# Performance work log

Hardware: AMD Instinct MI355X
Metric: run time of the kernel (lower is better)

Reference implementation:

```python
import jax, jax.numpy as jnp
import numpy as np

B, N, E, H, F, L, S = 4, 384, 768, 32, 3072, 12, 512
D = E // H


def setup_inputs() -> dict:
    key = jax.random.key(0)
    ks = jax.random.split(key, 32)
    inp = {}
    # forward args
    inp['node_type'] = jax.random.randint(ks[0], (B, N, 1), 1, S + 1)  # table has S+1 rows; 0 = pad (unused)
    inp['node_input_feature'] = jax.random.normal(ks[1], (B, N, E), jnp.float32)
    inp['in_degree'] = jax.random.randint(ks[2], (B, N), 0, S)
    inp['out_degree'] = jax.random.randint(ks[3], (B, N), 0, S)
    inp['attn_bias'] = jax.random.normal(ks[4], (B, N, N), jnp.float32) * 0.1
    inp['spatial_pos'] = jax.random.randint(ks[5], (B, N, N), 0, S)
    # embedding tables (normal stddev 0.02, as in the flax module)
    inp['node_emb'] = jax.random.normal(ks[6], (S + 1, E), jnp.float32) * 0.02
    inp['in_deg_emb'] = jax.random.normal(ks[7], (S, E), jnp.float32) * 0.02
    inp['out_deg_emb'] = jax.random.normal(ks[8], (S, E), jnp.float32) * 0.02
    inp['sp_emb'] = jax.random.normal(ks[9], (S, H), jnp.float32) * 0.02
    inp['sp_emb_rev'] = jax.random.normal(ks[10], (S, H), jnp.float32) * 0.02
    # per-layer weights, stacked along leading L axis
    se, sf = 1.0 / np.sqrt(E), 1.0 / np.sqrt(F)
    inp['Wq'] = jax.random.normal(ks[11], (L, E, E), jnp.float32) * se
    inp['bq'] = jax.random.normal(ks[12], (L, E), jnp.float32) * se
    inp['Wk'] = jax.random.normal(ks[13], (L, E, E), jnp.float32) * se
    inp['bk'] = jax.random.normal(ks[14], (L, E), jnp.float32) * se
    inp['Wv'] = jax.random.normal(ks[15], (L, E, E), jnp.float32) * se
    inp['bv'] = jax.random.normal(ks[16], (L, E), jnp.float32) * se
    inp['Wo'] = jax.random.normal(ks[17], (L, E, E), jnp.float32) * se
    inp['bo'] = jnp.zeros((L, E), jnp.float32)
    inp['W1'] = jax.random.normal(ks[18], (L, E, F), jnp.float32) * se
    inp['b1'] = jax.random.normal(ks[19], (L, F), jnp.float32) * se
    inp['W2'] = jax.random.normal(ks[20], (L, F, E), jnp.float32) * sf
    inp['b2'] = jax.random.normal(ks[21], (L, E), jnp.float32) * sf
    inp['ln1_s'] = jnp.ones((L, E), jnp.float32)
    inp['ln1_b'] = jnp.zeros((L, E), jnp.float32)
    inp['ln2_s'] = jnp.ones((L, E), jnp.float32)
    inp['ln2_b'] = jnp.zeros((L, E), jnp.float32)
    return inp


def _layernorm(x, scale, bias, eps=1e-5):
    m = x.mean(-1, keepdims=True)
    v = ((x - m) ** 2).mean(-1, keepdims=True)
    return (x - m) / jnp.sqrt(v + eps) * scale + bias


def _encoder(node_type, node_input_feature, in_degree, out_degree, attn_bias, spatial_pos,
             node_emb, in_deg_emb, out_deg_emb, sp_emb, sp_emb_rev,
             Wq, bq, Wk, bk, Wv, bv, Wo, bo, W1, b1, W2, b2, ln1_s, ln1_b, ln2_s, ln2_b):
    nt = node_type[..., 0]                               # [B,N]
    padding_mask = nt == 0                               # [B,N]
    # node features: node_emb(node_type).sum(-2) + degree embeddings + input feature
    x = (node_emb[node_type].sum(axis=-2)
         + in_deg_emb[in_degree] + out_deg_emb[out_degree]
         + node_input_feature)                           # [B,N,E]
    # spatial attention bias: [B,N,N,H] -> [B,H,N,N], plus graph-level attn_bias
    sb = sp_emb[spatial_pos] + sp_emb_rev[jnp.transpose(spatial_pos, (0, 2, 1))]
    bias = jnp.transpose(sb, (0, 3, 1, 2)) + attn_bias[:, None]  # [B,H,N,N]

    x = jnp.transpose(x, (1, 0, 2))                      # [N,B,E]
    scaling = D ** (-0.5)
    neg_inf = jnp.float32(-jnp.inf)

    def layer(x, p):
        wq, bq_, wk, bk_, wv, bv_, wo, bo_, w1, b1_, w2, b2_, s1, t1, s2, t2 = p
        q = ((x @ wq) + bq_) * scaling                   # [N,B,E], bias scaled too (faithful)
        k = (x @ wk) + bk_
        v = (x @ wv) + bv_
        q = q.reshape(N, B, H, D)
        k = k.reshape(N, B, H, D)
        v = v.reshape(N, B, H, D)
        w = jnp.einsum('nbhd,mbhd->bhnm', q, k) + bias   # [B,H,N,N]
        w = jnp.where(padding_mask[:, None, None, :], neg_inf, w)
        probs = jax.nn.softmax(w.astype(jnp.float32), axis=-1).astype(x.dtype)
        a = jnp.einsum('bhnm,mbhd->nbhd', probs, v).reshape(N, B, E)
        a = a @ wo + bo_
        x = _layernorm(x + a, s1, t1)                    # post-LN
        h = jax.nn.gelu(x @ w1 + b1_)                    # approximate gelu (flax default)
        h = h @ w2 + b2_
        x = _layernorm(x + h, s2, t2)
        return x, None

    xs = (Wq, bq, Wk, bk, Wv, bv, Wo, bo, W1, b1, W2, b2, ln1_s, ln1_b, ln2_s, ln2_b)
    x, _ = jax.lax.scan(layer, x, xs)
    return x                                             # [N,B,E]


def reference(node_type, node_input_feature, in_degree, out_degree, attn_bias, spatial_pos,
              node_emb, in_deg_emb, out_deg_emb, sp_emb, sp_emb_rev,
              Wq, bq, Wk, bk, Wv, bv, Wo, bo, W1, b1, W2, b2, ln1_s, ln1_b, ln2_s, ln2_b):
    return _encoder(node_type, node_input_feature, in_degree, out_degree, attn_bias, spatial_pos,
                    node_emb, in_deg_emb, out_deg_emb, sp_emb, sp_emb_rev,
                    Wq, bq, Wk, bk, Wv, bv, Wo, bo, W1, b1, W2, b2, ln1_s, ln1_b, ln2_s, ln2_b)
```

## Files before the change

kernel.cpp:

```cpp
#include <hip/hip_runtime.h>
#include <hip/hip_bf16.h>

#define Bb 4
#define Nn 384
#define Ee 768
#define Hh 32
#define Ff 3072
#define Ll 12
#define Ss 512
#define Mm (Nn*Bb)

typedef __attribute__((ext_vector_type(8))) short bf16x8;
typedef __attribute__((ext_vector_type(4))) float f32x4;
typedef unsigned short u16;

__device__ __forceinline__ u16 f2b(float f) {
  union { float f; unsigned int i; } c; c.f = f;
  unsigned int x = c.i;
  return (u16)((x + 0x7fffu + ((x >> 16) & 1u)) >> 16);
}
__device__ __forceinline__ float b2f(u16 u) {
  union { unsigned int i; float f; } c; c.i = ((unsigned int)u) << 16; return c.f;
}
__device__ __forceinline__ unsigned pkcvt(float lo, float hi) {
  unsigned r;
  asm("v_cvt_pk_bf16_f32 %0, %1, %2" : "=v"(r) : "v"(lo), "v"(hi));
  return r;
}
__device__ __forceinline__ void gload_lds16(const void* g, void* l) {
  __builtin_amdgcn_global_load_lds((__attribute__((address_space(1))) void*)(g),
                                   (__attribute__((address_space(3))) void*)(l), 16, 0, 0);
}

__global__ __launch_bounds__(256) void embed_kernel(
    const int* __restrict__ node_type, const float* __restrict__ nif,
    const int* __restrict__ in_deg, const int* __restrict__ out_deg,
    const float* __restrict__ node_emb, const float* __restrict__ ind_emb,
    const float* __restrict__ outd_emb,
    float* __restrict__ x, u16* __restrict__ xb)
{
  const int r = blockIdx.x;
  const int n = r / Bb, b = r % Bb;
  const int nt  = node_type[b*Nn + n];
  const int idg = in_deg[b*Nn + n];
  const int odg = out_deg[b*Nn + n];
  for (int c = threadIdx.x; c < Ee; c += 256) {
    float val = node_emb[(size_t)nt*Ee + c] + ind_emb[(size_t)idg*Ee + c]
              + outd_emb[(size_t)odg*Ee + c] + nif[((size_t)b*Nn + n)*Ee + c];
    x[(size_t)r*Ee + c] = val;
    xb[(size_t)r*Ee + c] = f2b(val);
  }
}

__global__ void spT_kernel(const int* __restrict__ sp, int* __restrict__ spT)
{
  __shared__ int tile[32][33];
  const int b = blockIdx.z;
  const int n0 = blockIdx.y * 32, m0 = blockIdx.x * 32;
  const int tx = threadIdx.x, ty = threadIdx.y;
  for (int i = ty; i < 32; i += 8)
    tile[i][tx] = sp[((size_t)b*Nn + n0 + i)*Nn + m0 + tx];
  __syncthreads();
  for (int i = ty; i < 32; i += 8)
    spT[((size_t)b*Nn + m0 + i)*Nn + n0 + tx] = tile[tx][i];
}

__global__ __launch_bounds__(256) void bias_pre_kernel(
    const float* __restrict__ atb, const int* __restrict__ sp, const int* __restrict__ spT,
    const float* __restrict__ sp_emb, const float* __restrict__ sp_emb_rev,
    u16* __restrict__ biasb)
{
  __shared__ float spc[512], sprc[512];
  const int bx = blockIdx.x, h = blockIdx.y, b = blockIdx.z;
  const int t = threadIdx.x;
  for (int i = t; i < 512; i += 256) {
    spc[i]  = sp_emb[(size_t)i*Hh + h];
    sprc[i] = sp_emb_rev[(size_t)i*Hh + h];
  }
  __syncthreads();
  const int qi = t >> 4;
  const int ml = (t & 15) << 2;
  const size_t rowb = ((size_t)b*Nn + bx*16 + qi)*Nn;
  u16* outb = biasb + ((size_t)(b*Hh + h)*24 + bx)*24*256;
  #pragma unroll
  for (int mg = 0; mg < 6; ++mg) {
    const int m = mg*64 + ml;
    float4 a4 = *(const float4*)(atb + rowb + m);
    int4  s4 = *(const int4*)(sp  + rowb + m);
    int4  t4 = *(const int4*)(spT + rowb + m);
    const int tt = m >> 4, hi = (m >> 2) & 3;
    uint2 u;
    u.x = pkcvt(a4.x + spc[s4.x] + sprc[t4.x], a4.y + spc[s4.y] + sprc[t4.y]);
    u.y = pkcvt(a4.z + spc[s4.z] + sprc[t4.z], a4.w + spc[s4.w] + sprc[t4.w]);
    *(uint2*)(outb + tt*256 + hi*64 + qi*4) = u;
  }
}

__global__ __launch_bounds__(256) void wconv_kernel(
    const float* __restrict__ Wq, const float* __restrict__ Wk, const float* __restrict__ Wv,
    const float* __restrict__ Wo, const float* __restrict__ W1, const float* __restrict__ W2,
    int layer, u16* __restrict__ slot)
{
  __shared__ float tile[64][65];
  int tid = blockIdx.x;
  const float* src; u16* dst; int Ns, Ks;
  if (tid < 432)       { int seg = tid / 144; tid -= seg*144;
                         src = (seg==0?Wq:(seg==1?Wk:Wv)) + (size_t)layer*Ee*Ee;
                         dst = slot + (size_t)seg*589824; Ns = 768; Ks = 768; }
  else if (tid < 576)  { tid -= 432; src = Wo + (size_t)layer*Ee*Ee; dst = slot + 1769472; Ns = 768;  Ks = 768; }
  else if (tid < 1152) { tid -= 576; src = W1 + (size_t)layer*Ee*Ff; dst = slot + 2359296; Ns = 3072; Ks = 768; }
  else                 { tid -= 1152; src = W2 + (size_t)layer*Ff*Ee; dst = slot + 4718592; Ns = 768; Ks = 3072; }
  const int tc = Ns >> 6;
  const int tk = tid / tc, tn = tid % tc;
  const int t = threadIdx.x;
  #pragma unroll
  for (int i = 0; i < 4; ++i) {
    const int id = t + i*256;
    const int r = id >> 4, c = (id & 15) << 2;
    float4 v = *(const float4*)(src + (size_t)(tk*64 + r)*Ns + tn*64 + c);
    tile[r][c+0] = v.x; tile[r][c+1] = v.y; tile[r][c+2] = v.z; tile[r][c+3] = v.w;
  }
  __syncthreads();
  #pragma unroll
  for (int i = 0; i < 2; ++i) {
    const int ch = t + i*256;
    const int n = ch >> 3, kc = (ch & 7) << 3;
    uint4 u;
    u.x = pkcvt(tile[kc+0][n], tile[kc+1][n]);
    u.y = pkcvt(tile[kc+2][n], tile[kc+3][n]);
    u.z = pkcvt(tile[kc+4][n], tile[kc+5][n]);
    u.w = pkcvt(tile[kc+6][n], tile[kc+7][n]);
    *(uint4*)(dst + (size_t)(tn*64 + n)*Ks + tk*64 + kc) = u;
  }
}

template<int EPI>
__global__ __launch_bounds__(256) void gemm3_kernel(
    const u16* __restrict__ A, const u16* __restrict__ Bw,
    const float* __restrict__ b0, const float* __restrict__ b1, const float* __restrict__ b2,
    int Kfull, int Kc, float scaleQ,
    float* __restrict__ outF, u16* __restrict__ outB)
{
  __shared__ __align__(16) u16 As[2][128][64];
  __shared__ __align__(16) u16 Bs[2][64][64];
  const int t = threadIdx.x, lane = t & 63, wave = t >> 6;
  int bx = blockIdx.x, by = blockIdx.y;
  {
    const int gx = gridDim.x;
    const int nwg = gx * gridDim.y;
    const int bid = bx + gx * by;
    const int cpx = nwg >> 3;
    const int s = (bid & 7) * cpx + (bid >> 3);
    bx = s % gx; by = s / gx;
  }
  const int m0 = bx * 128, n0 = by * 64;
  const int k0 = blockIdx.z * Kc;
  const int wm = wave >> 1, wn = wave & 1;
  const int ql = lane & 15, hi = lane >> 4;
  const int nk = Kc >> 6;
  const int sr = t >> 3;
  const int sslot = (t & 7) ^ (sr & 7);
  const size_t aoff = (size_t)(m0 + sr)*Kfull + k0 + (sslot << 3);
  const size_t boff = (size_t)(n0 + sr)*Kfull + k0 + (sslot << 3);
  const size_t rstep = (size_t)32 * Kfull;

  int aro[4][2], bro[2][2];
  #pragma unroll
  for (int ks = 0; ks < 2; ++ks) {
    const int kb = (((ks<<2) + hi) ^ (ql & 7)) << 4;
    #pragma unroll
    for (int f = 0; f < 4; ++f) aro[f][ks] = (wm*64 + f*16 + ql)*128 + kb;
    #pragma unroll
    for (int f = 0; f < 2; ++f) bro[f][ks] = (wn*32 + f*16 + ql)*128 + kb;
  }

  f32x4 acc[4][2];
  #pragma unroll
  for (int a = 0; a < 4; ++a)
    #pragma unroll
    for (int c = 0; c < 2; ++c) acc[a][c] = (f32x4){0.f,0.f,0.f,0.f};

  #pragma unroll
  for (int i = 0; i < 4; ++i)
    gload_lds16(A + aoff + i*rstep, (char*)&As[0][0][0] + i*4096 + t*16);
  #pragma unroll
  for (int i = 0; i < 2; ++i)
    gload_lds16(Bw + boff + i*rstep, (char*)&Bs[0][0][0] + i*4096 + t*16);

  for (int kt = 0; kt < nk; ++kt) {
    const int cur = kt & 1, nxt = cur ^ 1;
    const bool pre = (kt + 1 < nk);
    if (pre) {
      const size_t kk = (size_t)(kt + 1) << 6;
      #pragma unroll
      for (int i = 0; i < 4; ++i)
        gload_lds16(A + aoff + kk + i*rstep, (char*)&As[nxt][0][0] + i*4096 + t*16);
      #pragma unroll
      for (int i = 0; i < 2; ++i)
        gload_lds16(Bw + boff + kk + i*rstep, (char*)&Bs[nxt][0][0] + i*4096 + t*16);
      asm volatile("s_waitcnt vmcnt(6)" ::: "memory");
    } else {
      asm volatile("s_waitcnt vmcnt(0)" ::: "memory");
    }
    __builtin_amdgcn_s_barrier();
    __builtin_amdgcn_sched_barrier(0);

    const char* aBase = (const char*)&As[cur][0][0];
    const char* bBase = (const char*)&Bs[cur][0][0];
    bf16x8 af[4][2], bf[2][2];
    #pragma unroll
    for (int f = 0; f < 4; ++f)
      #pragma unroll
      for (int ks = 0; ks < 2; ++ks)
        af[f][ks] = *(const bf16x8*)(aBase + aro[f][ks]);
    #pragma unroll
    for (int f = 0; f < 2; ++f)
      #pragma unroll
      for (int ks = 0; ks < 2; ++ks)
        bf[f][ks] = *(const bf16x8*)(bBase + bro[f][ks]);
    #pragma unroll
    for (int ks = 0; ks < 2; ++ks)
      #pragma unroll
      for (int fm = 0; fm < 4; ++fm)
        #pragma unroll
        for (int fn = 0; fn < 2; ++fn)
          acc[fm][fn] = __builtin_amdgcn_mfma_f32_16x16x32_bf16(af[fm][ks], bf[fn][ks], acc[fm][fn], 0, 0, 0);
    if (pre) {
      __builtin_amdgcn_sched_barrier(0);
      __builtin_amdgcn_s_barrier();
    }
  }

  #pragma unroll
  for (int fm = 0; fm < 4; ++fm) {
    const int rowb = m0 + wm*64 + fm*16 + hi*4;
    #pragma unroll
    for (int fn = 0; fn < 2; ++fn) {
      const int gcol = n0 + wn*32 + fn*16 + ql;
      float bv, scale = 1.0f;
      if (EPI == 0) {
        const int seg = gcol / 768;
        const int cw = gcol - seg*768;
        bv = (seg == 0) ? b0[cw] : ((seg == 1) ? b1[cw] : b2[cw]);
        if (seg == 0) scale = scaleQ;
      } else if (EPI == 1) {
        bv = (blockIdx.z == 0) ? b0[gcol] : 0.0f;
      } else {
        bv = b0[gcol];
      }
      f32x4 v = acc[fm][fn];
      #pragma unroll
      for (int j = 0; j < 4; ++j) {
        float val = (v[j] + bv) * scale;
        if (EPI == 0) {
          outB[(size_t)(rowb + j) * 2304 + gcol] = f2b(val);
        } else if (EPI == 1) {
          outF[(size_t)blockIdx.z * (Mm*768) + (size_t)(rowb + j) * 768 + gcol] = val;
        } else {
          float arg = 0.7978845608028654f * (val + 0.044715f * val * val * val);
          float e = __expf(2.0f * arg);
          float g = 0.5f * val * (2.0f - 2.0f / (e + 1.0f));
          outB[(size_t)(rowb + j) * 3072 + gcol] = f2b(g);
        }
      }
    }
  }
}

template<int PREBIAS>
__global__ __launch_bounds__(256) void attn2_kernel(
    const u16* __restrict__ qkv,
    const u16* __restrict__ biasb,
    const float* __restrict__ atb, const int* __restrict__ sp, const int* __restrict__ spT,
    const float* __restrict__ sp_emb, const float* __restrict__ sp_emb_rev,
    u16* __restrict__ ab)
{
  __shared__ __align__(16) u16 Kt[384][32];
  __shared__ __align__(16) u16 Vt[32][392];
  __shared__ __align__(16) u16 Qt[64][32];
  __shared__ __align__(16) u16 Pw[4][16][32];
  __shared__ float spc[512], sprc[512];
  const int bid = blockIdx.x;
  const int pair = bid % 3;
  const int h = (bid / 3) % Hh;
  const int b = bid / (3 * Hh);
  const int t = threadIdx.x, lane = t & 63, wave = t >> 6;
  const int ql = lane & 15, hi = lane >> 4;

  for (int idx = t; idx < 384*6; idx += 256) {
    const int m = idx / 6, c = idx - m*6;
    const u16* base = qkv + ((size_t)m*Bb + b)*2304 + h*24 + c*4;
    uint2 kk = *(const uint2*)(base + 768);
    uint2 vv = *(const uint2*)(base + 1536);
    *(uint2*)&Kt[m][c*4] = kk;
    Vt[c*4+0][m] = (u16)(vv.x & 0xffffu); Vt[c*4+1][m] = (u16)(vv.x >> 16);
    Vt[c*4+2][m] = (u16)(vv.y & 0xffffu); Vt[c*4+3][m] = (u16)(vv.y >> 16);
  }
  for (int idx = t; idx < 384*2; idx += 256)
    *(uint2*)&Kt[idx>>1][24 + (idx&1)*4] = make_uint2(0u, 0u);
  for (int idx = t; idx < 8*196; idx += 256)
    *(unsigned*)((char*)&Vt[24][0] + idx*4) = 0u;
  for (int idx = t; idx < 64*2; idx += 256)
    *(uint2*)&Qt[idx>>1][24 + (idx&1)*4] = make_uint2(0u, 0u);
  if (!PREBIAS) {
    for (int i = t; i < 512; i += 256) {
      spc[i]  = sp_emb[(size_t)i*Hh + h];
      sprc[i] = sp_emb_rev[(size_t)i*Hh + h];
    }
  }

  for (int qi = 0; qi < 2; ++qi) {
    const int ntile = pair*2 + qi;
    for (int idx = t; idx < 64*6; idx += 256) {
      const int qr = idx / 6, c = idx - qr*6;
      const u16* base = qkv + ((size_t)(ntile*64 + qr)*Bb + b)*2304 + h*24 + c*4;
      *(uint2*)&Qt[qr][c*4] = *(const uint2*)base;
    }
    __syncthreads();

    const int q0 = ntile*64 + wave*16;
    const int q = q0 + ql;
    const bf16x8 qf = *(const bf16x8*)&Qt[wave*16 + ql][hi*8];

    f32x4 f[24];
    const u16* bp = biasb + (((size_t)(b*Hh + h)*24 + ntile*4 + wave)*24)*256 + lane*4;
    const size_t crow = ((size_t)b*Nn + q)*Nn;
    #pragma unroll
    for (int tt = 0; tt < 24; ++tt) {
      bf16x8 kf = *(const bf16x8*)&Kt[tt*16 + ql][hi*8];
      f32x4 z = (f32x4){0.f,0.f,0.f,0.f};
      f32x4 s = __builtin_amdgcn_mfma_f32_16x16x32_bf16(kf, qf, z, 0, 0, 0);
      if (PREBIAS) {
        uint2 bb = *(const uint2*)(bp + tt*256);
        s[0] += b2f((u16)(bb.x & 0xffffu)); s[1] += b2f((u16)(bb.x >> 16));
        s[2] += b2f((u16)(bb.y & 0xffffu)); s[3] += b2f((u16)(bb.y >> 16));
      } else {
        const int off = tt*16 + hi*4;
        int4 s4 = *(const int4*)(sp + crow + off);
        int4 t4 = *(const int4*)(spT + crow + off);
        float4 a4 = *(const float4*)(atb + crow + off);
        s[0] += a4.x + spc[s4.x] + sprc[t4.x];
        s[1] += a4.y + spc[s4.y] + sprc[t4.y];
        s[2] += a4.z + spc[s4.z] + sprc[t4.z];
        s[3] += a4.w + spc[s4.w] + sprc[t4.w];
      }
      f[tt] = s;
    }

    float mx = -3.0e38f;
    #pragma unroll
    for (int tt = 0; tt < 24; ++tt)
      mx = fmaxf(mx, fmaxf(fmaxf(f[tt][0], f[tt][1]), fmaxf(f[tt][2], f[tt][3])));
    mx = fmaxf(mx, __shfl_xor(mx, 16, 64));
    mx = fmaxf(mx, __shfl_xor(mx, 32, 64));
    float sum = 0.f;
    #pragma unroll
    for (int tt = 0; tt < 24; ++tt) {
      #pragma unroll
      for (int j = 0; j < 4; ++j) { f[tt][j] = __expf(f[tt][j] - mx); sum += f[tt][j]; }
    }
    sum += __shfl_xor(sum, 16, 64);
    sum += __shfl_xor(sum, 32, 64);
    const float inv = 1.0f / sum;

    f32x4 o0 = (f32x4){0.f,0.f,0.f,0.f}, o1 = (f32x4){0.f,0.f,0.f,0.f};
    char* prow = (char*)&Pw[wave][ql][0];
    const int swz = (ql & 3) << 4;
    #pragma unroll
    for (int c = 0; c < 12; ++c) {
      unsigned w0 = pkcvt(f[2*c][0],   f[2*c][1]);
      unsigned w1 = pkcvt(f[2*c][2],   f[2*c][3]);
      unsigned w2 = pkcvt(f[2*c+1][0], f[2*c+1][1]);
      unsigned w3 = pkcvt(f[2*c+1][2], f[2*c+1][3]);
      *(unsigned*)(prow + (((hi*8)      ) ^ swz)) = w0;
      *(unsigned*)(prow + (((hi*8) +  4) ^ swz)) = w1;
      *(unsigned*)(prow + (((hi*8) + 32) ^ swz)) = w2;
      *(unsigned*)(prow + (((hi*8) + 36) ^ swz)) = w3;
      bf16x8 a = *(const bf16x8*)(prow + ((hi*16) ^ swz));
      bf16x8 v0 = *(const bf16x8*)&Vt[ql][c*32 + hi*8];
      bf16x8 v1 = *(const bf16x8*)&Vt[16 + ql][c*32 + hi*8];
      o0 = __builtin_amdgcn_mfma_f32_16x16x32_bf16(a, v0, o0, 0, 0, 0);
      o1 = __builtin_amdgcn_mfma_f32_16x16x32_bf16(a, v1, o1, 0, 0, 0);
    }

    #pragma unroll
    for (int j = 0; j < 4; ++j) {
      float invj = __shfl(inv, hi*4 + j, 64);
      const int qg = q0 + hi*4 + j;
      u16* orow = ab + ((size_t)qg*Bb + b)*Ee + h*24;
      orow[ql] = f2b(o0[j] * invj);
      if (ql < 8) orow[16 + ql] = f2b(o1[j] * invj);
    }
    __syncthreads();
  }
}

template<int NP>
__global__ __launch_bounds__(256) void ln_kernel(
    const float* __restrict__ xin, const float* __restrict__ delta,
    const float* __restrict__ gamma, const float* __restrict__ beta,
    float* __restrict__ xout, u16* __restrict__ xb)
{
  const int wave = threadIdx.x >> 6, lane = threadIdx.x & 63;
  const int r = blockIdx.x * 4 + wave;
  const size_t base = (size_t)r * Ee;
  const int c0 = lane * 12;
  float v[12];
  #pragma unroll
  for (int i = 0; i < 3; ++i) {
    float4 xv = *(const float4*)(xin + base + c0 + i*4);
    v[i*4+0] = xv.x; v[i*4+1] = xv.y; v[i*4+2] = xv.z; v[i*4+3] = xv.w;
  }
  #pragma unroll
  for (int p = 0; p < NP; ++p) {
    const float* dp = delta + (size_t)p*(Mm*768) + base + c0;
    #pragma unroll
    for (int i = 0; i < 3; ++i) {
      float4 dv = *(const float4*)(dp + i*4);
      v[i*4+0] += dv.x; v[i*4+1] += dv.y; v[i*4+2] += dv.z; v[i*4+3] += dv.w;
    }
  }
  float s = 0.f;
  #pragma unroll
  for (int i = 0; i < 12; ++i) s += v[i];
  #pragma unroll
  for (int off = 1; off < 64; off <<= 1) s += __shfl_xor(s, off, 64);
  const float mean = s * (1.0f / 768.0f);
  float qs = 0.f;
  #pragma unroll
  for (int i = 0; i < 12; ++i) { float d = v[i] - mean; qs += d * d; }
  #pragma unroll
  for (int off = 1; off < 64; off <<= 1) qs += __shfl_xor(qs, off, 64);
  const float rstd = rsqrtf(qs * (1.0f / 768.0f) + 1e-5f);
  float o[12];
  #pragma unroll
  for (int i = 0; i < 3; ++i) {
    float4 g4 = *(const float4*)(gamma + c0 + i*4);
    float4 b4 = *(const float4*)(beta + c0 + i*4);
    o[i*4+0] = (v[i*4+0] - mean) * rstd * g4.x + b4.x;
    o[i*4+1] = (v[i*4+1] - mean) * rstd * g4.y + b4.y;
    o[i*4+2] = (v[i*4+2] - mean) * rstd * g4.z + b4.z;
    o[i*4+3] = (v[i*4+3] - mean) * rstd * g4.w + b4.w;
    *(float4*)(xout + base + c0 + i*4) = make_float4(o[i*4+0], o[i*4+1], o[i*4+2], o[i*4+3]);
  }
  #pragma unroll
  for (int i = 0; i < 3; ++i) {
    uint2 u;
    u.x = pkcvt(o[i*4+0], o[i*4+1]);
    u.y = pkcvt(o[i*4+2], o[i*4+3]);
    *(uint2*)(xb + base + c0 + i*4) = u;
  }
}

extern "C" void kernel_launch(void* const* d_in, const int* in_sizes, int n_in,
                              void* d_out, int out_size, void* d_ws, size_t ws_size,
                              hipStream_t stream) {
  const int*   node_type  = (const int*)d_in[0];
  const float* nif        = (const float*)d_in[1];
  const int*   in_deg     = (const int*)d_in[2];
  const int*   out_deg    = (const int*)d_in[3];
  const float* atb        = (const float*)d_in[4];
  const int*   sp         = (const int*)d_in[5];
  const float* node_emb   = (const float*)d_in[6];
  const float* ind_emb    = (const float*)d_in[7];
  const float* outd_emb   = (const float*)d_in[8];
  const float* sp_emb     = (const float*)d_in[9];
  const float* sp_emb_rev = (const float*)d_in[10];
  const float* Wq = (const float*)d_in[11]; const float* bq = (const float*)d_in[12];
  const float* Wk = (const float*)d_in[13]; const float* bk = (const float*)d_in[14];
  const float* Wv = (const float*)d_in[15]; const float* bv = (const float*)d_in[16];
  const float* Wo = (const float*)d_in[17]; const float* bo = (const float*)d_in[18];
  const float* W1 = (const float*)d_in[19]; const float* b1 = (const float*)d_in[20];
  const float* W2 = (const float*)d_in[21]; const float* b2 = (const float*)d_in[22];
  const float* ln1s = (const float*)d_in[23]; const float* ln1b = (const float*)d_in[24];
  const float* ln2s = (const float*)d_in[25]; const float* ln2b = (const float*)d_in[26];

  char* ws = (char*)d_ws;
  float* x      = (float*)(ws);
  u16*   xb     = (u16*)(ws +  4718592);
  u16*   qkvb16 = (u16*)(ws +  7077888);
  u16*   abuf   = (u16*)(ws + 14155776);
  u16*   hb     = (u16*)(ws + 16515072);
  float* obufP  = (float*)(ws + 25952256);
  int*   spTb   = (int*)(ws + 44826624);
  u16*   biasb  = (u16*)(ws + 47185920);
  u16*   wTslot = (u16*)(ws + 84934656);
  const bool useBias = ws_size >= 99090432ull;

  embed_kernel<<<Mm, 256, 0, stream>>>(node_type, nif, in_deg, out_deg,
                                       node_emb, ind_emb, outd_emb, x, xb);
  spT_kernel<<<dim3(12, 12, 4), dim3(32, 8), 0, stream>>>(sp, spTb);
  if (useBias)
    bias_pre_kernel<<<dim3(24, 32, 4), 256, 0, stream>>>(atb, sp, spTb, sp_emb, sp_emb_rev, biasb);

  const float scaleQ = 0.2041241452319315f;

  for (int l = 0; l < Ll; ++l) {
    const float *bql = bq + (size_t)l*Ee, *bkl = bk + (size_t)l*Ee, *bvl = bv + (size_t)l*Ee;
    const float *bol = bo + (size_t)l*Ee;
    const float *b1l = b1 + (size_t)l*Ff, *b2l = b2 + (size_t)l*Ee;

    wconv_kernel<<<1728, 256, 0, stream>>>(Wq, Wk, Wv, Wo, W1, W2, l, wTslot);
    const u16* qkvT = wTslot;
    const u16* woT  = wTslot + 1769472;
    const u16* w1T  = wTslot + 2359296;
    const u16* w2T  = wTslot + 4718592;

    gemm3_kernel<0><<<dim3(12, 36), 256, 0, stream>>>(xb, qkvT, bql, bkl, bvl,
                                                      768, 768, scaleQ, nullptr, qkvb16);
    if (useBias)
      attn2_kernel<1><<<384, 256, 0, stream>>>(qkvb16, biasb, atb, sp, spTb,
                                               sp_emb, sp_emb_rev, abuf);
    else
      attn2_kernel<0><<<384, 256, 0, stream>>>(qkvb16, nullptr, atb, sp, spTb,
                                               sp_emb, sp_emb_rev, abuf);
    gemm3_kernel<1><<<dim3(12, 12, 2), 256, 0, stream>>>(abuf, woT, bol, bol, bol,
                                                         768, 384, 1.0f, obufP, nullptr);
    ln_kernel<2><<<Mm/4, 256, 0, stream>>>(x, obufP, ln1s + (size_t)l*Ee, ln1b + (size_t)l*Ee, x, xb);
    gemm3_kernel<2><<<dim3(12, 48), 256, 0, stream>>>(xb, w1T, b1l, b1l, b1l,
                                                      768, 768, 1.0f, nullptr, hb);
    gemm3_kernel<1><<<dim3(12, 12, 4), 256, 0, stream>>>(hb, w2T, b2l, b2l, b2l,
                                                         3072, 768, 1.0f, obufP, nullptr);
    float* xdst = (l == Ll - 1) ? (float*)d_out : x;
    ln_kernel<4><<<Mm/4, 256, 0, stream>>>(x, obufP, ln2s + (size_t)l*Ee, ln2b + (size_t)l*Ee, xdst, xb);
  }
}
```

Measured before the change: 1.291 ms.

## Fuse fp32 weight conversion and transpose into GEMM B-tile loads

Drops the per-layer wconv kernel that converted and transposed fp32 weights to bf16 in a workspace slot. Each GEMM now reads fp32 weights directly from global memory into registers, packs them to bf16 and writes them swizzled into LDS. This removes one launch and a round trip through the workspace per layer. In exchange, B tiles are loaded as 4-byte strided scalar reads instead of async direct-to-LDS loads, M-tile blocks re-convert the same weights, and a __syncthreads replaces the vmcnt-based pipelining.

```diff
diff --git a/kernel.cpp b/kernel.cpp
--- a/kernel.cpp
+++ b/kernel.cpp
@@ -96,49 +96,12 @@
   }
 }
 
-__global__ __launch_bounds__(256) void wconv_kernel(
-    const float* __restrict__ Wq, const float* __restrict__ Wk, const float* __restrict__ Wv,
-    const float* __restrict__ Wo, const float* __restrict__ W1, const float* __restrict__ W2,
-    int layer, u16* __restrict__ slot)
-{
-  __shared__ float tile[64][65];
-  int tid = blockIdx.x;
-  const float* src; u16* dst; int Ns, Ks;
-  if (tid < 432)       { int seg = tid / 144; tid -= seg*144;
-                         src = (seg==0?Wq:(seg==1?Wk:Wv)) + (size_t)layer*Ee*Ee;
-                         dst = slot + (size_t)seg*589824; Ns = 768; Ks = 768; }
-  else if (tid < 576)  { tid -= 432; src = Wo + (size_t)layer*Ee*Ee; dst = slot + 1769472; Ns = 768;  Ks = 768; }
-  else if (tid < 1152) { tid -= 576; src = W1 + (size_t)layer*Ee*Ff; dst = slot + 2359296; Ns = 3072; Ks = 768; }
-  else                 { tid -= 1152; src = W2 + (size_t)layer*Ff*Ee; dst = slot + 4718592; Ns = 768; Ks = 3072; }
-  const int tc = Ns >> 6;
-  const int tk = tid / tc, tn = tid % tc;
-  const int t = threadIdx.x;
-  #pragma unroll
-  for (int i = 0; i < 4; ++i) {
-    const int id = t + i*256;
-    const int r = id >> 4, c = (id & 15) << 2;
-    float4 v = *(const float4*)(src + (size_t)(tk*64 + r)*Ns + tn*64 + c);
-    tile[r][c+0] = v.x; tile[r][c+1] = v.y; tile[r][c+2] = v.z; tile[r][c+3] = v.w;
-  }
-  __syncthreads();
-  #pragma unroll
-  for (int i = 0; i < 2; ++i) {
-    const int ch = t + i*256;
-    const int n = ch >> 3, kc = (ch & 7) << 3;
-    uint4 u;
-    u.x = pkcvt(tile[kc+0][n], tile[kc+1][n]);
-    u.y = pkcvt(tile[kc+2][n], tile[kc+3][n]);
-    u.z = pkcvt(tile[kc+4][n], tile[kc+5][n]);
-    u.w = pkcvt(tile[kc+6][n], tile[kc+7][n]);
-    *(uint4*)(dst + (size_t)(tn*64 + n)*Ks + tk*64 + kc) = u;
-  }
-}
-
 template<int EPI>
-__global__ __launch_bounds__(256) void gemm3_kernel(
-    const u16* __restrict__ A, const u16* __restrict__ Bw,
+__global__ __launch_bounds__(256) void gemm5_kernel(
+    const u16* __restrict__ A,
+    const float* __restrict__ W0, const float* __restrict__ W1p, const float* __restrict__ W2p,
     const float* __restrict__ b0, const float* __restrict__ b1, const float* __restrict__ b2,
-    int Kfull, int Kc, float scaleQ,
+    int Kfull, int Ns, int Kc, float scaleQ,
     float* __restrict__ outF, u16* __restrict__ outB)
 {
   __shared__ __align__(16) u16 As[2][128][64];
@@ -158,11 +121,20 @@
   const int wm = wave >> 1, wn = wave & 1;
   const int ql = lane & 15, hi = lane >> 4;
   const int nk = Kc >> 6;
+  int n0loc = n0;
+  const float* Wsel = W0;
+  if (EPI == 0) {
+    const int seg = n0 / 768; n0loc = n0 - seg*768;
+    Wsel = (seg == 0) ? W0 : ((seg == 1) ? W1p : W2p);
+  }
   const int sr = t >> 3;
   const int sslot = (t & 7) ^ (sr & 7);
   const size_t aoff = (size_t)(m0 + sr)*Kfull + k0 + (sslot << 3);
-  const size_t boff = (size_t)(n0 + sr)*Kfull + k0 + (sslot << 3);
   const size_t rstep = (size_t)32 * Kfull;
+  const int bn = t & 63, kq = t >> 6;
+  const float* wb = Wsel + (size_t)(k0 + kq*16)*Ns + n0loc + bn;
+  const int bws0 = ((kq*2)     ^ (bn & 7)) << 4;
+  const int bws1 = ((kq*2 + 1) ^ (bn & 7)) << 4;
 
   int aro[4][2], bro[2][2];
   #pragma unroll
@@ -180,30 +152,37 @@
     #pragma unroll
     for (int c = 0; c < 2; ++c) acc[a][c] = (f32x4){0.f,0.f,0.f,0.f};
 
-  #pragma unroll
-  for (int i = 0; i < 4; ++i)
-    gload_lds16(A + aoff + i*rstep, (char*)&As[0][0][0] + i*4096 + t*16);
-  #pragma unroll
-  for (int i = 0; i < 2; ++i)
-    gload_lds16(Bw + boff + i*rstep, (char*)&Bs[0][0][0] + i*4096 + t*16);
+  {
+    #pragma unroll
+    for (int i = 0; i < 4; ++i)
+      gload_lds16(A + aoff + i*rstep, (char*)&As[0][0][0] + i*4096 + t*16);
+    float br[16];
+    #pragma unroll
+    for (int i = 0; i < 16; ++i) br[i] = wb[(size_t)i * Ns];
+    uint4 u0, u1;
+    u0.x = pkcvt(br[0],  br[1]);  u0.y = pkcvt(br[2],  br[3]);
+    u0.z = pkcvt(br[4],  br[5]);  u0.w = pkcvt(br[6],  br[7]);
+    u1.x = pkcvt(br[8],  br[9]);  u1.y = pkcvt(br[10], br[11]);
+    u1.z = pkcvt(br[12], br[13]); u1.w = pkcvt(br[14], br[15]);
+    char* bdst = (char*)&Bs[0][0][0] + bn*128;
+    *(uint4*)(bdst + bws0) = u0;
+    *(uint4*)(bdst + bws1) = u1;
+  }
+  __syncthreads();
 
   for (int kt = 0; kt < nk; ++kt) {
     const int cur = kt & 1, nxt = cur ^ 1;
     const bool pre = (kt + 1 < nk);
+    float br[16];
     if (pre) {
       const size_t kk = (size_t)(kt + 1) << 6;
       #pragma unroll
       for (int i = 0; i < 4; ++i)
         gload_lds16(A + aoff + kk + i*rstep, (char*)&As[nxt][0][0] + i*4096 + t*16);
-      #pragma unroll
-      for (int i = 0; i < 2; ++i)
-        gload_lds16(Bw + boff + kk + i*rstep, (char*)&Bs[nxt][0][0] + i*4096 + t*16);
-      asm volatile("s_waitcnt vmcnt(6)" ::: "memory");
-    } else {
-      asm volatile("s_waitcnt vmcnt(0)" ::: "memory");
-    }
-    __builtin_amdgcn_s_barrier();
-    __builtin_amdgcn_sched_barrier(0);
+      const float* wbt = wb + kk * Ns;
+      #pragma unroll
+      for (int i = 0; i < 16; ++i) br[i] = wbt[(size_t)i * Ns];
+    }
 
     const char* aBase = (const char*)&As[cur][0][0];
     const char* bBase = (const char*)&Bs[cur][0][0];
@@ -225,9 +204,17 @@
         #pragma unroll
         for (int fn = 0; fn < 2; ++fn)
           acc[fm][fn] = __builtin_amdgcn_mfma_f32_16x16x32_bf16(af[fm][ks], bf[fn][ks], acc[fm][fn], 0, 0, 0);
+
     if (pre) {
-      __builtin_amdgcn_sched_barrier(0);
-      __builtin_amdgcn_s_barrier();
+      uint4 u0, u1;
+      u0.x = pkcvt(br[0],  br[1]);  u0.y = pkcvt(br[2],  br[3]);
+      u0.z = pkcvt(br[4],  br[5]);  u0.w = pkcvt(br[6],  br[7]);
+      u1.x = pkcvt(br[8],  br[9]);  u1.y = pkcvt(br[10], br[11]);
+      u1.z = pkcvt(br[12], br[13]); u1.w = pkcvt(br[14], br[15]);
+      char* bdst = (char*)&Bs[nxt][0][0] + bn*128;
+      *(uint4*)(bdst + bws0) = u0;
+      *(uint4*)(bdst + bws1) = u1;
+      __syncthreads();
     }
   }
 
@@ -484,7 +471,6 @@
   float* obufP  = (float*)(ws + 25952256);
   int*   spTb   = (int*)(ws + 44826624);
   u16*   biasb  = (u16*)(ws + 47185920);
-  u16*   wTslot = (u16*)(ws + 84934656);
   const bool useBias = ws_size >= 99090432ull;
 
   embed_kernel<<<Mm, 256, 0, stream>>>(node_type, nif, in_deg, out_deg,
@@ -496,31 +482,28 @@
   const float scaleQ = 0.2041241452319315f;
 
   for (int l = 0; l < Ll; ++l) {
+    const float *wq = Wq + (size_t)l*Ee*Ee, *wk = Wk + (size_t)l*Ee*Ee, *wv = Wv + (size_t)l*Ee*Ee;
+    const float *wo = Wo + (size_t)l*Ee*Ee;
+    const float *w1 = W1 + (size_t)l*Ee*Ff, *w2 = W2 + (size_t)l*Ff*Ee;
     const float *bql = bq + (size_t)l*Ee, *bkl = bk + (size_t)l*Ee, *bvl = bv + (size_t)l*Ee;
     const float *bol = bo + (size_t)l*Ee;
     const float *b1l = b1 + (size_t)l*Ff, *b2l = b2 + (size_t)l*Ee;
 
-    wconv_kernel<<<1728, 256, 0, stream>>>(Wq, Wk, Wv, Wo, W1, W2, l, wTslot);
-    const u16* qkvT = wTslot;
-    const u16* woT  = wTslot + 1769472;
-    const u16* w1T  = wTslot + 2359296;
-    const u16* w2T  = wTslot + 4718592;
-
-    gemm3_kernel<0><<<dim3(12, 36), 256, 0, stream>>>(xb, qkvT, bql, bkl, bvl,
-                                                      768, 768, scaleQ, nullptr, qkvb16);
+    gemm5_kernel<0><<<dim3(12, 36), 256, 0, stream>>>(xb, wq, wk, wv, bql, bkl, bvl,
+                                                      768, 768, 768, scaleQ, nullptr, qkvb16);
     if (useBias)
       attn2_kernel<1><<<384, 256, 0, stream>>>(qkvb16, biasb, atb, sp, spTb,
                                                sp_emb, sp_emb_rev, abuf);
     else
       attn2_kernel<0><<<384, 256, 0, stream>>>(qkvb16, nullptr, atb, sp, spTb,
                                                sp_emb, sp_emb_rev, abuf);
-    gemm3_kernel<1><<<dim3(12, 12, 2), 256, 0, stream>>>(abuf, woT, bol, bol, bol,
-                                                         768, 384, 1.0f, obufP, nullptr);
+    gemm5_kernel<1><<<dim3(12, 12, 2), 256, 0, stream>>>(abuf, wo, wo, wo, bol, bol, bol,
+                                                         768, 768, 384, 1.0f, obufP, nullptr);
     ln_kernel<2><<<Mm/4, 256, 0, stream>>>(x, obufP, ln1s + (size_t)l*Ee, ln1b + (size_t)l*Ee, x, xb);
-    gemm3_kernel<2><<<dim3(12, 48), 256, 0, stream>>>(xb, w1T, b1l, b1l, b1l,
-                                                      768, 768, 1.0f, nullptr, hb);
-    gemm3_kernel<1><<<dim3(12, 12, 4), 256, 0, stream>>>(hb, w2T, b2l, b2l, b2l,
-                                                         3072, 768, 1.0f, obufP, nullptr);
+    gemm5_kernel<2><<<dim3(12, 48), 256, 0, stream>>>(xb, w1, w1, w1, b1l, b1l, b1l,
+                                                      768, 3072, 768, 1.0f, nullptr, hb);
+    gemm5_kernel<1><<<dim3(12, 12, 4), 256, 0, stream>>>(hb, w2, w2, w2, b2l, b2l, b2l,
+                                                         3072, 768, 768, 1.0f, obufP, nullptr);
     float* xdst = (l == Ll - 1) ? (float*)d_out : x;
     ln_kernel<4><<<Mm/4, 256, 0, stream>>>(x, obufP, ln2s + (size_t)l*Ee, ln2b + (size_t)l*Ee, xdst, xb);
   }
```

After: 1.436 ms. 1.11x slower.

## Use 64-row GEMM tiles for Wo/W2, drop split-K, fold residual into epilogue

Applied to the files above, without the earlier changes.

Templates the GEMM on an M-fragment count so the Wo and W2 projections use 64-row tiles with more blocks in M. This replaces split-K 2 with no split for Wo and cuts W2 split-K from 4 to 2. The residual x is added in the split-0 epilogue, so the layernorm reads fewer partial buffers and no longer reads x separately. The aim is less partial-sum traffic and better occupancy, at the cost of lower per-block data reuse in the GEMM.

```diff
diff --git a/kernel.cpp b/kernel.cpp
--- a/kernel.cpp
+++ b/kernel.cpp
@@ -134,14 +134,16 @@
   }
 }
 
-template<int EPI>
+template<int EPI, int FM>
 __global__ __launch_bounds__(256) void gemm3_kernel(
     const u16* __restrict__ A, const u16* __restrict__ Bw,
     const float* __restrict__ b0, const float* __restrict__ b1, const float* __restrict__ b2,
+    const float* __restrict__ resid,
     int Kfull, int Kc, float scaleQ,
     float* __restrict__ outF, u16* __restrict__ outB)
 {
-  __shared__ __align__(16) u16 As[2][128][64];
+  constexpr int MR = FM * 32;
+  __shared__ __align__(16) u16 As[2][MR][64];
   __shared__ __align__(16) u16 Bs[2][64][64];
   const int t = threadIdx.x, lane = t & 63, wave = t >> 6;
   int bx = blockIdx.x, by = blockIdx.y;
@@ -153,7 +155,7 @@
     const int s = (bid & 7) * cpx + (bid >> 3);
     bx = s % gx; by = s / gx;
   }
-  const int m0 = bx * 128, n0 = by * 64;
+  const int m0 = bx * MR, n0 = by * 64;
   const int k0 = blockIdx.z * Kc;
   const int wm = wave >> 1, wn = wave & 1;
   const int ql = lane & 15, hi = lane >> 4;
@@ -164,24 +166,24 @@
   const size_t boff = (size_t)(n0 + sr)*Kfull + k0 + (sslot << 3);
   const size_t rstep = (size_t)32 * Kfull;
 
-  int aro[4][2], bro[2][2];
+  int aro[FM][2], bro[2][2];
   #pragma unroll
   for (int ks = 0; ks < 2; ++ks) {
     const int kb = (((ks<<2) + hi) ^ (ql & 7)) << 4;
     #pragma unroll
-    for (int f = 0; f < 4; ++f) aro[f][ks] = (wm*64 + f*16 + ql)*128 + kb;
+    for (int f = 0; f < FM; ++f) aro[f][ks] = (wm*(FM*16) + f*16 + ql)*128 + kb;
     #pragma unroll
     for (int f = 0; f < 2; ++f) bro[f][ks] = (wn*32 + f*16 + ql)*128 + kb;
   }
 
-  f32x4 acc[4][2];
-  #pragma unroll
-  for (int a = 0; a < 4; ++a)
+  f32x4 acc[FM][2];
+  #pragma unroll
+  for (int a = 0; a < FM; ++a)
     #pragma unroll
     for (int c = 0; c < 2; ++c) acc[a][c] = (f32x4){0.f,0.f,0.f,0.f};
 
   #pragma unroll
-  for (int i = 0; i < 4; ++i)
+  for (int i = 0; i < FM; ++i)
     gload_lds16(A + aoff + i*rstep, (char*)&As[0][0][0] + i*4096 + t*16);
   #pragma unroll
   for (int i = 0; i < 2; ++i)
@@ -193,12 +195,15 @@
     if (pre) {
       const size_t kk = (size_t)(kt + 1) << 6;
       #pragma unroll
-      for (int i = 0; i < 4; ++i)
+      for (int i = 0; i < FM; ++i)
         gload_lds16(A + aoff + kk + i*rstep, (char*)&As[nxt][0][0] + i*4096 + t*16);
       #pragma unroll
       for (int i = 0; i < 2; ++i)
         gload_lds16(Bw + boff + kk + i*rstep, (char*)&Bs[nxt][0][0] + i*4096 + t*16);
-      asm volatile("s_waitcnt vmcnt(6)" ::: "memory");
+      if constexpr (FM == 4)
+        asm volatile("s_waitcnt vmcnt(6)" ::: "memory");
+      else
+        asm volatile("s_waitcnt vmcnt(4)" ::: "memory");
     } else {
       asm volatile("s_waitcnt vmcnt(0)" ::: "memory");
     }
@@ -207,9 +212,9 @@
 
     const char* aBase = (const char*)&As[cur][0][0];
     const char* bBase = (const char*)&Bs[cur][0][0];
-    bf16x8 af[4][2], bf[2][2];
-    #pragma unroll
-    for (int f = 0; f < 4; ++f)
+    bf16x8 af[FM][2], bf[2][2];
+    #pragma unroll
+    for (int f = 0; f < FM; ++f)
       #pragma unroll
       for (int ks = 0; ks < 2; ++ks)
         af[f][ks] = *(const bf16x8*)(aBase + aro[f][ks]);
@@ -221,7 +226,7 @@
     #pragma unroll
     for (int ks = 0; ks < 2; ++ks)
       #pragma unroll
-      for (int fm = 0; fm < 4; ++fm)
+      for (int fm = 0; fm < FM; ++fm)
         #pragma unroll
         for (int fn = 0; fn < 2; ++fn)
           acc[fm][fn] = __builtin_amdgcn_mfma_f32_16x16x32_bf16(af[fm][ks], bf[fn][ks], acc[fm][fn], 0, 0, 0);
@@ -232,8 +237,8 @@
   }
 
   #pragma unroll
-  for (int fm = 0; fm < 4; ++fm) {
-    const int rowb = m0 + wm*64 + fm*16 + hi*4;
+  for (int fm = 0; fm < FM; ++fm) {
+    const int rowb = m0 + wm*(FM*16) + fm*16 + hi*4;
     #pragma unroll
     for (int fn = 0; fn < 2; ++fn) {
       const int gcol = n0 + wn*32 + fn*16 + ql;
@@ -255,6 +260,7 @@
         if (EPI == 0) {
           outB[(size_t)(rowb + j) * 2304 + gcol] = f2b(val);
         } else if (EPI == 1) {
+          if (blockIdx.z == 0) val += resid[(size_t)(rowb + j) * 768 + gcol];
           outF[(size_t)blockIdx.z * (Mm*768) + (size_t)(rowb + j) * 768 + gcol] = val;
         } else {
           float arg = 0.7978845608028654f * (val + 0.044715f * val * val * val);
@@ -397,7 +403,7 @@
 
 template<int NP>
 __global__ __launch_bounds__(256) void ln_kernel(
-    const float* __restrict__ xin, const float* __restrict__ delta,
+    const float* __restrict__ delta,
     const float* __restrict__ gamma, const float* __restrict__ beta,
     float* __restrict__ xout, u16* __restrict__ xb)
 {
@@ -407,10 +413,7 @@
   const int c0 = lane * 12;
   float v[12];
   #pragma unroll
-  for (int i = 0; i < 3; ++i) {
-    float4 xv = *(const float4*)(xin + base + c0 + i*4);
-    v[i*4+0] = xv.x; v[i*4+1] = xv.y; v[i*4+2] = xv.z; v[i*4+3] = xv.w;
-  }
+  for (int i = 0; i < 12; ++i) v[i] = 0.f;
   #pragma unroll
   for (int p = 0; p < NP; ++p) {
     const float* dp = delta + (size_t)p*(Mm*768) + base + c0;
@@ -506,22 +509,22 @@
     const u16* w1T  = wTslot + 2359296;
     const u16* w2T  = wTslot + 4718592;
 
-    gemm3_kernel<0><<<dim3(12, 36), 256, 0, stream>>>(xb, qkvT, bql, bkl, bvl,
-                                                      768, 768, scaleQ, nullptr, qkvb16);
+    gemm3_kernel<0,4><<<dim3(12, 36), 256, 0, stream>>>(xb, qkvT, bql, bkl, bvl, nullptr,
+                                                        768, 768, scaleQ, nullptr, qkvb16);
     if (useBias)
       attn2_kernel<1><<<384, 256, 0, stream>>>(qkvb16, biasb, atb, sp, spTb,
                                                sp_emb, sp_emb_rev, abuf);
     else
       attn2_kernel<0><<<384, 256, 0, stream>>>(qkvb16, nullptr, atb, sp, spTb,
                                                sp_emb, sp_emb_rev, abuf);
-    gemm3_kernel<1><<<dim3(12, 12, 2), 256, 0, stream>>>(abuf, woT, bol, bol, bol,
-                                                         768, 384, 1.0f, obufP, nullptr);
-    ln_kernel<2><<<Mm/4, 256, 0, stream>>>(x, obufP, ln1s + (size_t)l*Ee, ln1b + (size_t)l*Ee, x, xb);
-    gemm3_kernel<2><<<dim3(12, 48), 256, 0, stream>>>(xb, w1T, b1l, b1l, b1l,
-                                                      768, 768, 1.0f, nullptr, hb);
-    gemm3_kernel<1><<<dim3(12, 12, 4), 256, 0, stream>>>(hb, w2T, b2l, b2l, b2l,
-                                                         3072, 768, 1.0f, obufP, nullptr);
+    gemm3_kernel<1,2><<<dim3(24, 12), 256, 0, stream>>>(abuf, woT, bol, bol, bol, x,
+                                                        768, 768, 1.0f, obufP, nullptr);
+    ln_kernel<1><<<Mm/4, 256, 0, stream>>>(obufP, ln1s + (size_t)l*Ee, ln1b + (size_t)l*Ee, x, xb);
+    gemm3_kernel<2,4><<<dim3(12, 48), 256, 0, stream>>>(xb, w1T, b1l, b1l, b1l, nullptr,
+                                                        768, 768, 1.0f, nullptr, hb);
+    gemm3_kernel<1,2><<<dim3(24, 12, 2), 256, 0, stream>>>(hb, w2T, b2l, b2l, b2l, x,
+                                                           3072, 1536, 1.0f, obufP, nullptr);
     float* xdst = (l == Ll - 1) ? (float*)d_out : x;
-    ln_kernel<4><<<Mm/4, 256, 0, stream>>>(x, obufP, ln2s + (size_t)l*Ee, ln2b + (size_t)l*Ee, xdst, xb);
-  }
-}
+    ln_kernel<2><<<Mm/4, 256, 0, stream>>>(obufP, ln2s + (size_t)l*Ee, ln2b + (size_t)l*Ee, xdst, xb);
+  }
+}
```

After: 1.382 ms. 1.07x slower.
